# Kernel tuning notes

Hardware: AMD Instinct MI355X
Metric: run time of the kernel (lower is better)

The kernel has to match this reference:

```python
import jax, jax.numpy as jnp
import numpy as np

EPS = 1e-5
NUM_HEADS = 8
KEY_DEPTH = 128   # base_filters * key_expansion
VAL_DEPTH = 256   # base_filters * value_expansion
C_IN = 256


def conv1x1(x, w):
    # x: [N, Cin, L], w: [Cout, Cin] (1x1 conv, no bias)
    return jnp.einsum('oc,ncl->nol', w, x)


def group_norm1(x, w, b, eps=EPS):
    # torch GroupNorm(1, C) on [N, C, L]: normalize over (C, L) per sample,
    # per-channel affine.
    mu = jnp.mean(x, axis=(1, 2), keepdims=True)
    var = jnp.var(x, axis=(1, 2), keepdims=True)
    xn = (x - mu) * jax.lax.rsqrt(var + eps)
    return xn * w[None, :, None] + b[None, :, None]


def layer_norm_last2(x, eps=EPS):
    # freshly-constructed nn.LayerNorm([A, B]): weight=1, bias=0 -> pure norm
    mu = jnp.mean(x, axis=(-2, -1), keepdims=True)
    var = jnp.var(x, axis=(-2, -1), keepdims=True)
    return (x - mu) * jax.lax.rsqrt(var + eps)


def gelu(x):
    return jax.nn.gelu(x, approximate=False)  # torch F.gelu default (erf)


def setup_inputs() -> dict:
    key = jax.random.key(0)
    ks = jax.random.split(key, 16)
    N, L = 8, 1024
    qkv_out = 2 * KEY_DEPTH + VAL_DEPTH  # 512

    def w(k, shape, std=0.02):
        return jax.random.normal(k, shape, jnp.float32) * std

    def gw(k, c):
        return 1.0 + 0.1 * jax.random.normal(k, (c,), jnp.float32)

    return {
        'f': jax.random.normal(ks[0], (N, C_IN, L), jnp.float32),
        'w_z': w(ks[1], (C_IN, C_IN), np.sqrt(2.0 / C_IN)),
        'gz_w': gw(ks[2], C_IN), 'gz_b': w(ks[3], (C_IN,)),
        'w_qkv': w(ks[4], (qkv_out, C_IN), C_IN ** -0.5),
        'gq_w': gw(ks[5], qkv_out), 'gq_b': w(ks[6], (qkv_out,)),
        'w_out': w(ks[7], (C_IN, VAL_DEPTH), np.sqrt(2.0 / VAL_DEPTH)),
        'go_w': gw(ks[8], C_IN), 'go_b': w(ks[9], (C_IN,)),
        'w_ffn1': w(ks[10], (2 * C_IN, C_IN), np.sqrt(2.0 / C_IN)),
        'g1_w': gw(ks[11], 2 * C_IN), 'g1_b': w(ks[12], (2 * C_IN,)),
        'w_ffn2': w(ks[13], (C_IN, 2 * C_IN), np.sqrt(1.0 / C_IN)),
        'g2_w': gw(ks[14], C_IN), 'g2_b': w(ks[15], (C_IN,)),
    }


def reference(f, w_z, gz_w, gz_b, w_qkv, gq_w, gq_b, w_out, go_w, go_b,
              w_ffn1, g1_w, g1_b, w_ffn2, g2_w, g2_b):
    N, C, L = f.shape
    H = NUM_HEADS

    z = gelu(group_norm1(conv1x1(gelu(f), w_z), gz_w, gz_b))
    qkv = group_norm1(conv1x1(z, w_qkv), gq_w, gq_b)
    q, k, v = jnp.split(qkv, [KEY_DEPTH, 2 * KEY_DEPTH], axis=1)
    q = q.reshape(N, H, KEY_DEPTH // H, L)
    k = k.reshape(N, H, KEY_DEPTH // H, L)
    v = v.reshape(N, H, VAL_DEPTH // H, L)

    # [N, H, L, L] similarity, no scaling, then LayerNorm over full LxL map
    logits = jnp.einsum('nhcl,nhcm->nhlm', q, k)
    logits = layer_norm_last2(logits)

    # scatter-mask: diagonal -> -inf for every head
    eye = jnp.eye(L, dtype=bool)[None, None]  # [1,1,L,L]
    logits = jnp.where(eye, -jnp.inf, logits)

    attn = jax.nn.softmax(logits.astype(jnp.float32), axis=-1)
    attn = jnp.where(jnp.isnan(attn), 0.0, attn)

    out = jnp.einsum('nhlm,nhdm->nhdl', attn, v).reshape(N, VAL_DEPTH, L)
    out = gelu(layer_norm_last2(out))  # LayerNorm([C_v, L]), fresh params

    out = group_norm1(conv1x1(out, w_out), go_w, go_b)
    f = gelu(f + out)

    h = gelu(group_norm1(conv1x1(f, w_ffn1), g1_w, g1_b))
    h = group_norm1(conv1x1(h, w_ffn2), g2_w, g2_b)
    return gelu(f + h)
```

## Files before the change

kernel.cpp:

```cpp
#include <hip/hip_runtime.h>

#define LSEQ 1024

typedef __attribute__((ext_vector_type(8))) short bf16x8;
typedef __attribute__((ext_vector_type(4))) float f32x4;

__device__ __forceinline__ float gelu_f(float x){
    return 0.5f*x*(1.0f+erff(x*0.7071067811865476f));
}

__device__ __forceinline__ unsigned cvtpk(float lo, float hi){
    unsigned r;
    asm("v_cvt_pk_bf16_f32 %0, %1, %2" : "=v"(r) : "v"(lo), "v"(hi));
    return r;
}

__global__ __launch_bounds__(256,2) void prologue(
    const float* __restrict__ w0, const float* __restrict__ w1,
    const float* __restrict__ w2, const float* __restrict__ w3,
    const float* __restrict__ w4, unsigned short* __restrict__ wdst,
    const float* __restrict__ f, unsigned short* __restrict__ t0,
    float* __restrict__ stats, float* __restrict__ covs,
    unsigned* __restrict__ kmaxu)
{
    __shared__ float T[64][68];
    int b = blockIdx.x;
    int tid = threadIdx.x;

    if(b < 512){
        int ltile = (b&15)*64, ctile = ((b>>4)&3)*64, n = b>>6;
        const float* s = f + (size_t)n*256*LSEQ;
        int cl = tid>>4, l4 = (tid&15)*4;
        #pragma unroll
        for(int p=0;p<4;p++){
            int c_loc = p*16 + cl;
            float4 v = *(const float4*)&s[(size_t)(ctile+c_loc)*LSEQ + ltile + l4];
            float4 t;
            t.x = gelu_f(v.x); t.y = gelu_f(v.y); t.z = gelu_f(v.z); t.w = gelu_f(v.w);
            *(float4*)&T[c_loc][l4] = t;
        }
        __syncthreads();
        int l_loc = tid>>2, cg = (tid&3)*16;
        uint4 o0, o1;
        o0.x = cvtpk(T[cg+0][l_loc],  T[cg+1][l_loc]);
        o0.y = cvtpk(T[cg+2][l_loc],  T[cg+3][l_loc]);
        o0.z = cvtpk(T[cg+4][l_loc],  T[cg+5][l_loc]);
        o0.w = cvtpk(T[cg+6][l_loc],  T[cg+7][l_loc]);
        o1.x = cvtpk(T[cg+8][l_loc],  T[cg+9][l_loc]);
        o1.y = cvtpk(T[cg+10][l_loc], T[cg+11][l_loc]);
        o1.z = cvtpk(T[cg+12][l_loc], T[cg+13][l_loc]);
        o1.w = cvtpk(T[cg+14][l_loc], T[cg+15][l_loc]);
        unsigned short* d = t0 + (size_t)n*LSEQ*256 + (size_t)(ltile+l_loc)*256 + ctile + cg;
        *(uint4*)d = o0;
        *(uint4*)(d+8) = o1;
    } else if(b < 1024){
        int idx4 = (b-512)*256 + tid;
        const float* src; int off4;
        if(idx4 < 16384){ src=w0; off4=idx4; }
        else if(idx4 < 49152){ src=w1; off4=idx4-16384; }
        else if(idx4 < 65536){ src=w2; off4=idx4-49152; }
        else if(idx4 < 98304){ src=w3; off4=idx4-65536; }
        else { src=w4; off4=idx4-98304; }
        float4 v = ((const float4*)src)[off4];
        uint2 p; p.x = cvtpk(v.x,v.y); p.y = cvtpk(v.z,v.w);
        ((uint2*)wdst)[idx4] = p;
    } else if(b == 1024){
        if(tid < 64) ((float4*)stats)[tid] = (float4){0.f,0.f,0.f,0.f};
        if(tid >= 64 && tid < 80) ((uint4*)kmaxu)[tid-64] = (uint4){0,0,0,0};
    } else {
        int i = (b-1025)*256 + tid;
        ((float4*)covs)[i] = (float4){0.f,0.f,0.f,0.f};
    }
}

__global__ __launch_bounds__(256,2) void xform_bf16(
    const float* __restrict__ src, const float* __restrict__ res,
    const float* __restrict__ stats,
    const float* __restrict__ gw, const float* __restrict__ gb,
    float cnt_inv, int C, unsigned short* __restrict__ dst)
{
    __shared__ float T[64][68];
    int n = blockIdx.z;
    int ltile = blockIdx.x*64, ctile = blockIdx.y*64;
    int tid = threadIdx.x;

    float mu=0.f, istd=1.f;
    if(stats){
        float s1 = stats[2*n], s2 = stats[2*n+1];
        mu = s1*cnt_inv;
        istd = rsqrtf(s2*cnt_inv - mu*mu + 1e-5f);
    }
    const float* s = src + (size_t)n*C*LSEQ;
    const float* r = res ? res + (size_t)n*C*LSEQ : nullptr;

    int cl = tid>>4, l4 = (tid&15)*4;
    #pragma unroll
    for(int p=0;p<4;p++){
        int c_loc = p*16 + cl;
        int c = ctile + c_loc;
        float w_ = 1.f, b_ = 0.f;
        if(stats){ w_ = istd; b_ = -mu*istd; }
        if(gw){ b_ = gb[c] + b_*gw[c]; w_ *= gw[c]; }
        float4 v = *(const float4*)&s[(size_t)c*LSEQ + ltile + l4];
        float4 t;
        t.x = v.x*w_+b_; t.y = v.y*w_+b_; t.z = v.z*w_+b_; t.w = v.w*w_+b_;
        if(r){
            float4 rv = *(const float4*)&r[(size_t)c*LSEQ + ltile + l4];
            t.x += rv.x; t.y += rv.y; t.z += rv.z; t.w += rv.w;
        }
        t.x = gelu_f(t.x); t.y = gelu_f(t.y); t.z = gelu_f(t.z); t.w = gelu_f(t.w);
        *(float4*)&T[c_loc][l4] = t;
    }
    __syncthreads();

    int l_loc = tid>>2, cg = (tid&3)*16;
    uint4 o0, o1;
    o0.x = cvtpk(T[cg+0][l_loc],  T[cg+1][l_loc]);
    o0.y = cvtpk(T[cg+2][l_loc],  T[cg+3][l_loc]);
    o0.z = cvtpk(T[cg+4][l_loc],  T[cg+5][l_loc]);
    o0.w = cvtpk(T[cg+6][l_loc],  T[cg+7][l_loc]);
    o1.x = cvtpk(T[cg+8][l_loc],  T[cg+9][l_loc]);
    o1.y = cvtpk(T[cg+10][l_loc], T[cg+11][l_loc]);
    o1.z = cvtpk(T[cg+12][l_loc], T[cg+13][l_loc]);
    o1.w = cvtpk(T[cg+14][l_loc], T[cg+15][l_loc]);
    unsigned short* d = dst + (size_t)n*LSEQ*C + (size_t)(ltile+l_loc)*C + ctile + cg;
    *(uint4*)d = o0;
    *(uint4*)(d+8) = o1;
}

__global__ __launch_bounds__(256,4) void gemm_bf16(
    const unsigned short* __restrict__ Abf,
    const unsigned short* __restrict__ Bbf,
    float* __restrict__ C,
    int M, int K,
    float* __restrict__ out_stats)
{
    __shared__ short Bs[64*264];

    int tid = threadIdx.x;
    int n = blockIdx.z, n0 = blockIdx.x*64, m0 = blockIdx.y*64;
    int wave = tid>>6, lane = tid&63;
    int col = lane&15, quad = lane>>4;
    int srow = tid>>2, sks = (tid&3)*8;

    const unsigned short* apt = Abf + (size_t)(m0+wave*16+col)*K + quad*8;
    const unsigned short* bpt = Bbf + ((size_t)n*LSEQ + n0+srow)*K + sks;

    f32x4 acc[4];
    #pragma unroll
    for(int t=0;t<4;t++) acc[t] = (f32x4){0.f,0.f,0.f,0.f};

    for(int kp=0; kp<K; kp+=256){
        __syncthreads();
        uint4 bw[8];
        #pragma unroll
        for(int i=0;i<8;i++) bw[i] = *(const uint4*)(bpt + kp + i*32);
        #pragma unroll
        for(int i=0;i<8;i++) *(uint4*)&Bs[srow*264 + sks + i*32] = bw[i];
        __syncthreads();

        #pragma unroll
        for(int kc=0;kc<8;kc++){
            bf16x8 af = *(const bf16x8*)(apt + kp + kc*32);
            #pragma unroll
            for(int t=0;t<4;t++){
                bf16x8 bf = *(bf16x8*)&Bs[(t*16+col)*264 + kc*32 + quad*8];
                acc[t] = __builtin_amdgcn_mfma_f32_16x16x32_bf16(af, bf, acc[t], 0,0,0);
            }
        }
    }

    __syncthreads();
    size_t cbase = (size_t)n*M*LSEQ;
    float lsum=0.f, lsq=0.f;
    #pragma unroll
    for(int t=0;t<4;t++){
        #pragma unroll
        for(int r2=0;r2<4;r2++){
            int m = m0 + wave*16 + quad*4 + r2;
            int l = n0 + t*16 + col;
            float v = acc[t][r2];
            C[cbase + (size_t)m*LSEQ + l] = v;
            lsum += v; lsq += v*v;
        }
    }
    #pragma unroll
    for(int d=1;d<64;d<<=1){
        lsum += __shfl_xor(lsum, d);
        lsq  += __shfl_xor(lsq,  d);
    }
    float* scr = (float*)Bs;
    if(lane==0){ scr[wave] = lsum; scr[8+wave] = lsq; }
    __syncthreads();
    if(tid==0){
        atomicAdd(&out_stats[2*n],   (scr[0]+scr[1])+(scr[2]+scr[3]));
        atomicAdd(&out_stats[2*n+1], (scr[8]+scr[9])+(scr[10]+scr[11]));
    }
}

__global__ __launch_bounds__(256,4) void gemm_bf16_m128(
    const unsigned short* __restrict__ Abf,
    const unsigned short* __restrict__ Bbf,
    float* __restrict__ C,
    int M, int K,
    float* __restrict__ out_stats)
{
    __shared__ short Bs[64*264];

    int tid = threadIdx.x;
    int n = blockIdx.z, n0 = blockIdx.x*64, m0 = blockIdx.y*128;
    int wave = tid>>6, lane = tid&63;
    int col = lane&15, quad = lane>>4;
    int srow = tid>>2, sks = (tid&3)*8;

    const unsigned short* apt0 = Abf + (size_t)(m0+wave*32+col)*K + quad*8;
    const unsigned short* apt1 = apt0 + (size_t)16*K;
    const unsigned short* bpt = Bbf + ((size_t)n*LSEQ + n0+srow)*K + sks;

    f32x4 acc[2][4];
    #pragma unroll
    for(int mf=0;mf<2;mf++)
        #pragma unroll
        for(int t=0;t<4;t++) acc[mf][t] = (f32x4){0.f,0.f,0.f,0.f};

    for(int kp=0; kp<K; kp+=256){
        __syncthreads();
        uint4 bw[8];
        #pragma unroll
        for(int i=0;i<8;i++) bw[i] = *(const uint4*)(bpt + kp + i*32);
        #pragma unroll
        for(int i=0;i<8;i++) *(uint4*)&Bs[srow*264 + sks + i*32] = bw[i];
        __syncthreads();

        #pragma unroll
        for(int kc=0;kc<8;kc++){
            bf16x8 af0 = *(const bf16x8*)(apt0 + kp + kc*32);
            bf16x8 af1 = *(const bf16x8*)(apt1 + kp + kc*32);
            #pragma unroll
            for(int t=0;t<4;t++){
                bf16x8 bf = *(bf16x8*)&Bs[(t*16+col)*264 + kc*32 + quad*8];
                acc[0][t] = __builtin_amdgcn_mfma_f32_16x16x32_bf16(af0, bf, acc[0][t], 0,0,0);
                acc[1][t] = __builtin_amdgcn_mfma_f32_16x16x32_bf16(af1, bf, acc[1][t], 0,0,0);
            }
        }
    }

    __syncthreads();
    size_t cbase = (size_t)n*M*LSEQ;
    float lsum=0.f, lsq=0.f;
    #pragma unroll
    for(int mf=0;mf<2;mf++){
        #pragma unroll
        for(int t=0;t<4;t++){
            #pragma unroll
            for(int r2=0;r2<4;r2++){
                int m = m0 + wave*32 + mf*16 + quad*4 + r2;
                int l = n0 + t*16 + col;
                float v = acc[mf][t][r2];
                C[cbase + (size_t)m*LSEQ + l] = v;
                lsum += v; lsq += v*v;
            }
        }
    }
    #pragma unroll
    for(int d=1;d<64;d<<=1){
        lsum += __shfl_xor(lsum, d);
        lsq  += __shfl_xor(lsq,  d);
    }
    float* scr = (float*)Bs;
    if(lane==0){ scr[wave] = lsum; scr[8+wave] = lsq; }
    __syncthreads();
    if(tid==0){
        atomicAdd(&out_stats[2*n],   (scr[0]+scr[1])+(scr[2]+scr[3]));
        atomicAdd(&out_stats[2*n+1], (scr[8]+scr[9])+(scr[10]+scr[11]));
    }
}

__global__ __launch_bounds__(256,2) void head_cov(
    const float* __restrict__ qkv,
    const float* __restrict__ s_qkv,
    const float* __restrict__ gq_w, const float* __restrict__ gq_b,
    float* __restrict__ covq, float* __restrict__ covk,
    float* __restrict__ sumq, float* __restrict__ sumk,
    unsigned short* __restrict__ Qbf, unsigned short* __restrict__ Kbf,
    unsigned short* __restrict__ Vbf,
    float* __restrict__ qnorm, unsigned* __restrict__ kmaxu)
{
    __shared__ float Kq[16*132];
    __shared__ float Kk[16*132];
    int b = blockIdx.x;
    int head = b>>3, chunk = b&7;
    int n = head>>3, h = head&7;
    int tid = threadIdx.x;
    int m0 = chunk*128;

    float s1 = s_qkv[2*n], s2v = s_qkv[2*n+1];
    float mu  = s1*(1.f/524288.f);
    float var = s2v*(1.f/524288.f) - mu*mu;
    float istd = rsqrtf(var + 1e-5f);

    const float* base = qkv + (size_t)n*512*LSEQ;
    int m = tid&127, cg = tid>>7;
    #pragma unroll
    for(int cc=0;cc<8;cc++){
        int c = cg*8+cc;
        int chq = h*16+c, chk = 128+h*16+c;
        Kq[c*132+m] = (base[(size_t)chq*LSEQ+m0+m]-mu)*istd*gq_w[chq]+gq_b[chq];
        Kk[c*132+m] = (base[(size_t)chk*LSEQ+m0+m]-mu)*istd*gq_w[chk]+gq_b[chk];
    }

    {
        int d = tid>>3, mg = tid&7;
        int ch = 256 + h*32 + d;
        float vw = gq_w[ch]*istd, vb = gq_b[ch]-mu*istd*gq_w[ch];
        const float* vs = base + (size_t)ch*LSEQ + m0 + mg*16;
        float4 a0 = *(const float4*)&vs[0];
        float4 a1 = *(const float4*)&vs[4];
        float4 a2 = *(const float4*)&vs[8];
        float4 a3 = *(const float4*)&vs[12];
        uint4 p0, p1;
        p0.x = cvtpk(a0.x*vw+vb, a0.y*vw+vb);
        p0.y = cvtpk(a0.z*vw+vb, a0.w*vw+vb);
        p0.z = cvtpk(a1.x*vw+vb, a1.y*vw+vb);
        p0.w = cvtpk(a1.z*vw+vb, a1.w*vw+vb);
        p1.x = cvtpk(a2.x*vw+vb, a2.y*vw+vb);
        p1.y = cvtpk(a2.z*vw+vb, a2.w*vw+vb);
        p1.z = cvtpk(a3.x*vw+vb, a3.y*vw+vb);
        p1.w = cvtpk(a3.z*vw+vb, a3.w*vw+vb);
        unsigned short* dv = Vbf + ((size_t)head*32 + d)*1024 + m0 + mg*16;
        *(uint4*)dv = p0;
        *(uint4*)(dv+8) = p1;
    }
    __syncthreads();

    int i = tid>>4, j = tid&15;
    float q0=0,q1=0,q2=0,q3=0, k0=0,k1=0,k2=0,k3=0;
    for(int mm=0;mm<128;mm+=4){
        float4 qa = *(const float4*)&Kq[i*132+mm];
        float4 qb = *(const float4*)&Kq[j*132+mm];
        q0 += qa.x*qb.x; q1 += qa.y*qb.y; q2 += qa.z*qb.z; q3 += qa.w*qb.w;
        float4 ka = *(const float4*)&Kk[i*132+mm];
        float4 kb = *(const float4*)&Kk[j*132+mm];
        k0 += ka.x*kb.x; k1 += ka.y*kb.y; k2 += ka.z*kb.z; k3 += ka.w*kb.w;
    }
    atomicAdd(&covq[head*256 + i*16 + j], (q0+q1)+(q2+q3));
    atomicAdd(&covk[head*256 + i*16 + j], (k0+k1)+(k2+k3));

    if(i==0){
        float s=0.f;
        for(int mm=0;mm<128;mm+=4){
            float4 v = *(const float4*)&Kq[j*132+mm];
            s += (v.x+v.y)+(v.z+v.w);
        }
        atomicAdd(&sumq[head*16+j], s);
    }
    if(i==1){
        float s=0.f;
        for(int mm=0;mm<128;mm+=4){
            float4 v = *(const float4*)&Kk[j*132+mm];
            s += (v.x+v.y)+(v.z+v.w);
        }
        atomicAdd(&sumk[head*16+j], s);
    }

    {
        int mm2 = tid & 127;
        if(tid < 128){
            unsigned u[8]; float s2 = 0.f;
            #pragma unroll
            for(int c=0;c<16;c+=2){
                float a = Kq[c*132+mm2], b2 = Kq[(c+1)*132+mm2];
                s2 += a*a + b2*b2;
                u[c>>1] = cvtpk(a, b2);
            }
            unsigned short* dq = Qbf + ((size_t)head*1024 + m0 + mm2)*16;
            *(uint4*)dq     = *(uint4*)&u[0];
            *(uint4*)(dq+8) = *(uint4*)&u[4];
            qnorm[head*1024 + m0 + mm2] = s2;
        } else {
            unsigned u[8]; float s2 = 0.f;
            #pragma unroll
            for(int c=0;c<16;c+=2){
                float a = Kk[c*132+mm2], b2 = Kk[(c+1)*132+mm2];
                s2 += a*a + b2*b2;
                u[c>>1] = cvtpk(a, b2);
            }
            unsigned short* dk = Kbf + ((size_t)head*1024 + m0 + mm2)*16;
            *(uint4*)dk     = *(uint4*)&u[0];
            *(uint4*)(dk+8) = *(uint4*)&u[4];
            #pragma unroll
            for(int d=1;d<64;d<<=1) s2 = fmaxf(s2, __shfl_xor(s2, d));
            if((tid&63)==0) atomicMax(kmaxu + head, __float_as_uint(s2));
        }
    }
}

__global__ __launch_bounds__(256) void attn_kernel(
    const unsigned short* __restrict__ Qbf,
    const unsigned short* __restrict__ Kbf,
    const unsigned short* __restrict__ Vbf,
    const float* __restrict__ qnorm, const unsigned* __restrict__ kmaxu,
    const float* __restrict__ covq, const float* __restrict__ covk,
    const float* __restrict__ sumq, const float* __restrict__ sumk,
    float* __restrict__ out,
    float* __restrict__ out_stats)
{
    __shared__ short Qs[128*40];
    __shared__ short Ks[128*40];
    __shared__ short Vs[32*136];
    __shared__ short Ps[128*152];
    __shared__ float bounds_l[128];
    __shared__ float issum_l[128];
    __shared__ float sred4[4];

    int b = blockIdx.x;
    int head = b&63, rb = b>>6;
    int n = head>>3, h = head&7;
    int tid = threadIdx.x;
    int wv = tid>>6, lane = tid&63;
    int col = lane&15, quad = lane>>4;
    int l0 = rb*128;

    float ih;
    {
        float prod = covq[head*256+tid]*covk[head*256+tid];
        #pragma unroll
        for(int d=1;d<64;d<<=1) prod += __shfl_xor(prod, d);
        if(lane==0) sred4[wv] = prod;
        __syncthreads();
        if(tid==0){
            double S2 = (double)sred4[0] + (double)sred4[1]
                      + (double)sred4[2] + (double)sred4[3];
            double S1 = 0.0;
            for(int c=0;c<16;c++)
                S1 += (double)sumq[head*16+c]*(double)sumk[head*16+c];
            double cnt = 1048576.0;
            double mean = S1/cnt;
            double v2 = S2/cnt - mean*mean;
            if(v2 < 0.0) v2 = 0.0;
            sred4[0] = (float)(1.0/sqrt(v2 + 1e-5));
        }
        __syncthreads();
        ih = sred4[0];
    }
    float ihl = ih * 1.4426950408889634f;

    {
        uint4 z = {0,0,0,0};
        int row = tid>>1, hf = tid&1;
        *(uint4*)&Ks[row*40 + 16 + hf*8] = z;
        *(uint4*)&Qs[row*40 + 16 + hf*8] = z;
        const unsigned short* qsrc = Qbf + ((size_t)head*1024 + l0 + row)*16 + hf*8;
        *(uint4*)&Qs[row*40 + hf*8] = *(const uint4*)qsrc;
        if(tid < 128) bounds_l[tid] = sqrtf(qnorm[head*1024 + l0 + tid]);
    }
    float kmax = sqrtf(__uint_as_float(kmaxu[head]));
    __syncthreads();

    bf16x8 qf[2];
    float B2l[2]; int grow[2];
    #pragma unroll
    for(int t=0;t<2;t++){
        int rl = (2*wv+t)*16 + col;
        qf[t] = *(bf16x8*)&Qs[rl*40 + quad*8];
        B2l[t] = bounds_l[rl]*kmax*ihl;
        grow[t] = l0 + rl;
    }

    int krow = tid>>1, khalf = tid&1;
    const unsigned short* ksrc = Kbf + ((size_t)head*1024 + krow)*16 + khalf*8;
    int vdd = tid>>3, vmg = tid&7;
    const unsigned short* vsrc = Vbf + ((size_t)head*32 + vdd)*1024 + vmg*16;

    f32x4 acc[2][2];
    #pragma unroll
    for(int t=0;t<2;t++){ acc[t][0]=(f32x4){0,0,0,0}; acc[t][1]=(f32x4){0,0,0,0}; }
    float ssum[2] = {0.f,0.f};
    const f32x4 zero4 = {0.f,0.f,0.f,0.f};

    uint4 kreg = *(const uint4*)ksrc;
    uint4 vr0  = *(const uint4*)vsrc;
    uint4 vr1  = *(const uint4*)(vsrc + 8);

    for(int mc=0;mc<8;mc++){
        int M0 = mc*128;
        *(uint4*)&Ks[krow*40 + khalf*8]    = kreg;
        *(uint4*)&Vs[vdd*136 + vmg*16]     = vr0;
        *(uint4*)&Vs[vdd*136 + vmg*16 + 8] = vr1;
        __syncthreads();

        if(mc < 7){
            kreg = *(const uint4*)(ksrc + (size_t)(M0+128)*16);
            vr0  = *(const uint4*)(vsrc + M0+128);
            vr1  = *(const uint4*)(vsrc + M0+136);
        }

        __builtin_amdgcn_s_setprio(1);
        bool dg = (mc == rb);
        #pragma unroll
        for(int mt=0;mt<8;mt++){
            bf16x8 ak = *(bf16x8*)&Ks[(mt*16+col)*40 + quad*8];
            #pragma unroll
            for(int t=0;t<2;t++){
                f32x4 sc = __builtin_amdgcn_mfma_f32_16x16x32_bf16(ak, qf[t], zero4, 0,0,0);
                float pr[4];
                #pragma unroll
                for(int r=0;r<4;r++)
                    pr[r] = exp2f(fmaf(sc[r], ihl, -B2l[t]));
                if(dg){
                    int mbase = M0 + mt*16 + quad*4;
                    #pragma unroll
                    for(int r=0;r<4;r++)
                        if(mbase + r == grow[t]) pr[r] = 0.f;
                }
                ssum[t] += (pr[0]+pr[1])+(pr[2]+pr[3]);
                uint2 pw;
                pw.x = cvtpk(pr[0],pr[1]); pw.y = cvtpk(pr[2],pr[3]);
                *(uint2*)&Ps[((2*wv+t)*16+col)*152 + mt*16 + quad*4] = pw;
            }
        }
        #pragma unroll
        for(int kk=0;kk<4;kk++){
            bf16x8 bv0 = *(bf16x8*)&Vs[( col)*136 + kk*32 + quad*8];
            bf16x8 bv1 = *(bf16x8*)&Vs[(16+col)*136 + kk*32 + quad*8];
            #pragma unroll
            for(int t=0;t<2;t++){
                bf16x8 ap = *(bf16x8*)&Ps[((2*wv+t)*16+col)*152 + kk*32 + quad*8];
                acc[t][0] = __builtin_amdgcn_mfma_f32_16x16x32_bf16(ap, bv0, acc[t][0], 0,0,0);
                acc[t][1] = __builtin_amdgcn_mfma_f32_16x16x32_bf16(ap, bv1, acc[t][1], 0,0,0);
            }
        }
        __builtin_amdgcn_s_setprio(0);
        __syncthreads();
    }

    #pragma unroll
    for(int t=0;t<2;t++){
        float v = ssum[t];
        v += __shfl_xor(v,16);
        v += __shfl_xor(v,32);
        if(quad==0) issum_l[(2*wv+t)*16+col] = v;
    }
    __syncthreads();
    if(tid<128) issum_l[tid] = 1.f/issum_l[tid];
    __syncthreads();

    float* ep = (float*)Ps;
    #pragma unroll
    for(int t=0;t<2;t++)
        #pragma unroll
        for(int dt=0;dt<2;dt++)
            *(f32x4*)&ep[(dt*16+col)*132 + (2*wv+t)*16 + quad*4] = acc[t][dt];
    __syncthreads();

    float lsum=0.f, lsq=0.f;
    size_t obase = (size_t)n*262144 + (size_t)h*32*LSEQ + l0;
    #pragma unroll
    for(int t=0;t<16;t++){
        int idx = t*256 + tid;
        int d = idx>>7, row = idx&127;
        float y = ep[d*132+row]*issum_l[row];
        out[obase + (size_t)d*LSEQ + row] = y;
        lsum += y; lsq += y*y;
    }
    float* red = (float*)Ks;
    red[tid]=lsum; red[256+tid]=lsq;
    __syncthreads();
    for(int s=128;s>0;s>>=1){
        if(tid<s){ red[tid]+=red[tid+s]; red[256+tid]+=red[256+tid+s]; }
        __syncthreads();
    }
    if(tid==0){
        atomicAdd(&out_stats[2*n],   red[0]);
        atomicAdd(&out_stats[2*n+1], red[256]);
    }
}

__global__ __launch_bounds__(256) void ew_final(
    const float* __restrict__ f, const float* __restrict__ x,
    const float* __restrict__ h2,
    const float* __restrict__ sx, const float* __restrict__ sh,
    const float* __restrict__ go_w, const float* __restrict__ go_b,
    const float* __restrict__ g2_w, const float* __restrict__ g2_b,
    float* __restrict__ out)
{
    int idx = blockIdx.x*256 + threadIdx.x;
    int n = idx >> 16;
    int c = (idx >> 8) & 255;
    float mux, isx, muh, ish;
    {
        float s1 = sx[2*n], s2 = sx[2*n+1];
        mux = s1*(1.f/262144.f);
        isx = rsqrtf(s2*(1.f/262144.f) - mux*mux + 1e-5f);
        float t1 = sh[2*n], t2 = sh[2*n+1];
        muh = t1*(1.f/262144.f);
        ish = rsqrtf(t2*(1.f/262144.f) - muh*muh + 1e-5f);
    }
    float wo = go_w[c]*isx, bo = go_b[c]-mux*isx*go_w[c];
    float w2 = g2_w[c]*ish, b2 = g2_b[c]-muh*ish*g2_w[c];
    float4 xv = ((const float4*)x)[idx];
    float4 fv = ((const float4*)f)[idx];
    float4 hv = ((const float4*)h2)[idx];
    float4 ov;
    float f1;
    f1 = gelu_f(fv.x + xv.x*wo+bo); ov.x = gelu_f(f1 + hv.x*w2+b2);
    f1 = gelu_f(fv.y + xv.y*wo+bo); ov.y = gelu_f(f1 + hv.y*w2+b2);
    f1 = gelu_f(fv.z + xv.z*wo+bo); ov.z = gelu_f(f1 + hv.z*w2+b2);
    f1 = gelu_f(fv.w + xv.w*wo+bo); ov.w = gelu_f(f1 + hv.w*w2+b2);
    ((float4*)out)[idx] = ov;
}

extern "C" void kernel_launch(void* const* d_in, const int* in_sizes, int n_in,
                              void* d_out, int out_size, void* d_ws, size_t ws_size,
                              hipStream_t stream) {
    const float* f     = (const float*)d_in[0];
    const float* w_z   = (const float*)d_in[1];
    const float* gz_w  = (const float*)d_in[2];
    const float* gz_b  = (const float*)d_in[3];
    const float* w_qkv = (const float*)d_in[4];
    const float* gq_w  = (const float*)d_in[5];
    const float* gq_b  = (const float*)d_in[6];
    const float* w_out = (const float*)d_in[7];
    const float* go_w  = (const float*)d_in[8];
    const float* go_b  = (const float*)d_in[9];
    const float* w_f1  = (const float*)d_in[10];
    const float* g1_w  = (const float*)d_in[11];
    const float* g1_b  = (const float*)d_in[12];
    const float* w_f2  = (const float*)d_in[13];
    const float* g2_w  = (const float*)d_in[14];
    const float* g2_b  = (const float*)d_in[15];

    float* ws = (float*)d_ws;
    float* stats = ws;
    float* s_z    = stats + 0;
    float* s_qkv  = stats + 16;
    float* s_attn = stats + 32;
    float* s_x    = stats + 48;
    float* s_h1   = stats + 64;
    float* s_h2   = stats + 80;

    float* qkvF = ws + 256;
    float* z0F  = qkvF + 4194304;
    float* xF   = z0F + 2097152;
    unsigned short* t0 = (unsigned short*)(xF + 2097152);
    unsigned short* t1 = t0 + 2097152;
    unsigned short* wp = t1 + 2097152;
    unsigned short* t4 = (unsigned short*)z0F;
    unsigned short* wp_z   = wp;
    unsigned short* wp_qkv = wp + 65536;
    unsigned short* wp_out = wp + 196608;
    unsigned short* wp_f1  = wp + 262144;
    unsigned short* wp_f2  = wp + 393216;

    float* covq = xF;
    float* covk = xF + 16384;
    float* sumq = xF + 32768;
    float* sumk = xF + 33792;
    float* qnorm = xF + 34816;
    unsigned* kmaxu = (unsigned*)(xF + 100352);

    unsigned short* Qbf = t0;
    unsigned short* Kbf = t0 + 1048576;
    unsigned short* Vbf = t1;

    float* outp = (float*)d_out;

    dim3 blk(256);
    prologue<<<1059,blk,0,stream>>>(w_z, w_qkv, w_out, w_f1, w_f2, wp,
        f, t0, stats, covq, kmaxu);
    gemm_bf16<<<dim3(16,4,8),blk,0,stream>>>(wp_z, t0, z0F, 256, 256, s_z);
    xform_bf16<<<dim3(16,4,8),blk,0,stream>>>(z0F, nullptr, s_z, gz_w, gz_b,
        1.f/262144.f, 256, t1);
    gemm_bf16_m128<<<dim3(16,4,8),blk,0,stream>>>(wp_qkv, t1, qkvF, 512, 256, s_qkv);
    head_cov<<<512,blk,0,stream>>>(qkvF, s_qkv, gq_w, gq_b, covq, covk, sumq, sumk,
        Qbf, Kbf, Vbf, qnorm, kmaxu);
    attn_kernel<<<512,blk,0,stream>>>(Qbf, Kbf, Vbf, qnorm, kmaxu,
        covq, covk, sumq, sumk, z0F, s_attn);
    xform_bf16<<<dim3(16,4,8),blk,0,stream>>>(z0F, nullptr, s_attn, nullptr, nullptr,
        1.f/262144.f, 256, t0);
    gemm_bf16<<<dim3(16,4,8),blk,0,stream>>>(wp_out, t0, xF, 256, 256, s_x);
    xform_bf16<<<dim3(16,4,8),blk,0,stream>>>(xF, f, s_x, go_w, go_b,
        1.f/262144.f, 256, t1);
    gemm_bf16_m128<<<dim3(16,4,8),blk,0,stream>>>(wp_f1, t1, qkvF, 512, 256, s_h1);
    xform_bf16<<<dim3(16,8,8),blk,0,stream>>>(qkvF, nullptr, s_h1, g1_w, g1_b,
        1.f/524288.f, 512, t4);
    gemm_bf16<<<dim3(16,4,8),blk,0,stream>>>(wp_f2, t4, qkvF, 256, 512, s_h2);
    ew_final<<<2048,blk,0,stream>>>(f, xF, qkvF, s_x, s_h2,
        go_w, go_b, g2_w, g2_b, outp);
}
```

Before: 279.4 us.

## Fuse norm+GELU+bf16 transpose staging into GEMM B-tile loads

Removes the separate xform_bf16 passes and the gelu prologue transpose. Each GEMM now reads the fp32 activation directly, applies the group-norm affine, optional residual and GELU, and transposes through shared memory into the bf16 B tile. This saves several launches and the write and read of the bf16 intermediates. In exchange, every M-tile block recomputes GELU/erf for the same B columns (4x or 2x redundancy), adds extra barriers and LDS, and occupancy drops to 3 blocks per CU.

```diff
diff --git a/kernel.cpp b/kernel.cpp
--- a/kernel.cpp
+++ b/kernel.cpp
@@ -15,46 +15,66 @@
     return r;
 }
 
+__device__ __forceinline__ void stage_B_fused(
+    short* Bs, float* T,
+    const float* __restrict__ src, const float* __restrict__ res,
+    const float* __restrict__ gw, const float* __restrict__ gb,
+    float mu, float istd, bool has_stats,
+    int n0, int kp, int tid)
+{
+    int cl = tid>>4, l4 = (tid&15)*4;
+    int l_loc = tid>>2, cg = (tid&3)*16;
+    #pragma unroll
+    for(int sub=0; sub<4; sub++){
+        int cbase = kp + sub*64;
+        float4 tv[4];
+        #pragma unroll
+        for(int p=0;p<4;p++){
+            int c = cbase + p*16 + cl;
+            float w_ = 1.f, b_ = 0.f;
+            if(has_stats){ w_ = istd; b_ = -mu*istd; }
+            if(gw){ b_ = gb[c] + b_*gw[c]; w_ *= gw[c]; }
+            float4 v = *(const float4*)&src[(size_t)c*LSEQ + n0 + l4];
+            float4 t;
+            t.x = v.x*w_+b_; t.y = v.y*w_+b_; t.z = v.z*w_+b_; t.w = v.w*w_+b_;
+            if(res){
+                float4 rv = *(const float4*)&res[(size_t)c*LSEQ + n0 + l4];
+                t.x += rv.x; t.y += rv.y; t.z += rv.z; t.w += rv.w;
+            }
+            t.x = gelu_f(t.x); t.y = gelu_f(t.y); t.z = gelu_f(t.z); t.w = gelu_f(t.w);
+            tv[p] = t;
+        }
+        __syncthreads();
+        #pragma unroll
+        for(int p=0;p<4;p++) *(float4*)&T[(p*16+cl)*68 + l4] = tv[p];
+        __syncthreads();
+        uint4 o0, o1;
+        o0.x = cvtpk(T[(cg+0)*68+l_loc],  T[(cg+1)*68+l_loc]);
+        o0.y = cvtpk(T[(cg+2)*68+l_loc],  T[(cg+3)*68+l_loc]);
+        o0.z = cvtpk(T[(cg+4)*68+l_loc],  T[(cg+5)*68+l_loc]);
+        o0.w = cvtpk(T[(cg+6)*68+l_loc],  T[(cg+7)*68+l_loc]);
+        o1.x = cvtpk(T[(cg+8)*68+l_loc],  T[(cg+9)*68+l_loc]);
+        o1.y = cvtpk(T[(cg+10)*68+l_loc], T[(cg+11)*68+l_loc]);
+        o1.z = cvtpk(T[(cg+12)*68+l_loc], T[(cg+13)*68+l_loc]);
+        o1.w = cvtpk(T[(cg+14)*68+l_loc], T[(cg+15)*68+l_loc]);
+        *(uint4*)&Bs[l_loc*264 + sub*64 + cg]     = o0;
+        *(uint4*)&Bs[l_loc*264 + sub*64 + cg + 8] = o1;
+    }
+    __syncthreads();
+}
+
 __global__ __launch_bounds__(256,2) void prologue(
     const float* __restrict__ w0, const float* __restrict__ w1,
     const float* __restrict__ w2, const float* __restrict__ w3,
     const float* __restrict__ w4, unsigned short* __restrict__ wdst,
-    const float* __restrict__ f, unsigned short* __restrict__ t0,
     float* __restrict__ stats, float* __restrict__ covs,
     unsigned* __restrict__ kmaxu)
 {
-    __shared__ float T[64][68];
     int b = blockIdx.x;
     int tid = threadIdx.x;
 
     if(b < 512){
-        int ltile = (b&15)*64, ctile = ((b>>4)&3)*64, n = b>>6;
-        const float* s = f + (size_t)n*256*LSEQ;
-        int cl = tid>>4, l4 = (tid&15)*4;
-        #pragma unroll
-        for(int p=0;p<4;p++){
-            int c_loc = p*16 + cl;
-            float4 v = *(const float4*)&s[(size_t)(ctile+c_loc)*LSEQ + ltile + l4];
-            float4 t;
-            t.x = gelu_f(v.x); t.y = gelu_f(v.y); t.z = gelu_f(v.z); t.w = gelu_f(v.w);
-            *(float4*)&T[c_loc][l4] = t;
-        }
-        __syncthreads();
-        int l_loc = tid>>2, cg = (tid&3)*16;
-        uint4 o0, o1;
-        o0.x = cvtpk(T[cg+0][l_loc],  T[cg+1][l_loc]);
-        o0.y = cvtpk(T[cg+2][l_loc],  T[cg+3][l_loc]);
-        o0.z = cvtpk(T[cg+4][l_loc],  T[cg+5][l_loc]);
-        o0.w = cvtpk(T[cg+6][l_loc],  T[cg+7][l_loc]);
-        o1.x = cvtpk(T[cg+8][l_loc],  T[cg+9][l_loc]);
-        o1.y = cvtpk(T[cg+10][l_loc], T[cg+11][l_loc]);
-        o1.z = cvtpk(T[cg+12][l_loc], T[cg+13][l_loc]);
-        o1.w = cvtpk(T[cg+14][l_loc], T[cg+15][l_loc]);
-        unsigned short* d = t0 + (size_t)n*LSEQ*256 + (size_t)(ltile+l_loc)*256 + ctile + cg;
-        *(uint4*)d = o0;
-        *(uint4*)(d+8) = o1;
-    } else if(b < 1024){
-        int idx4 = (b-512)*256 + tid;
+        int idx4 = b*256 + tid;
         const float* src; int off4;
         if(idx4 < 16384){ src=w0; off4=idx4; }
         else if(idx4 < 49152){ src=w1; off4=idx4-16384; }
@@ -64,100 +84,50 @@
         float4 v = ((const float4*)src)[off4];
         uint2 p; p.x = cvtpk(v.x,v.y); p.y = cvtpk(v.z,v.w);
         ((uint2*)wdst)[idx4] = p;
-    } else if(b == 1024){
+    } else if(b == 512){
         if(tid < 64) ((float4*)stats)[tid] = (float4){0.f,0.f,0.f,0.f};
         if(tid >= 64 && tid < 80) ((uint4*)kmaxu)[tid-64] = (uint4){0,0,0,0};
     } else {
-        int i = (b-1025)*256 + tid;
+        int i = (b-513)*256 + tid;
         ((float4*)covs)[i] = (float4){0.f,0.f,0.f,0.f};
     }
 }
 
-__global__ __launch_bounds__(256,2) void xform_bf16(
-    const float* __restrict__ src, const float* __restrict__ res,
-    const float* __restrict__ stats,
+__global__ __launch_bounds__(256,3) void gemm_fused(
+    const unsigned short* __restrict__ Abf,
+    const float* __restrict__ srcF, const float* __restrict__ resF,
+    const float* __restrict__ in_stats, float cnt_inv, int Csrc,
     const float* __restrict__ gw, const float* __restrict__ gb,
-    float cnt_inv, int C, unsigned short* __restrict__ dst)
-{
-    __shared__ float T[64][68];
-    int n = blockIdx.z;
-    int ltile = blockIdx.x*64, ctile = blockIdx.y*64;
-    int tid = threadIdx.x;
-
-    float mu=0.f, istd=1.f;
-    if(stats){
-        float s1 = stats[2*n], s2 = stats[2*n+1];
-        mu = s1*cnt_inv;
-        istd = rsqrtf(s2*cnt_inv - mu*mu + 1e-5f);
-    }
-    const float* s = src + (size_t)n*C*LSEQ;
-    const float* r = res ? res + (size_t)n*C*LSEQ : nullptr;
-
-    int cl = tid>>4, l4 = (tid&15)*4;
-    #pragma unroll
-    for(int p=0;p<4;p++){
-        int c_loc = p*16 + cl;
-        int c = ctile + c_loc;
-        float w_ = 1.f, b_ = 0.f;
-        if(stats){ w_ = istd; b_ = -mu*istd; }
-        if(gw){ b_ = gb[c] + b_*gw[c]; w_ *= gw[c]; }
-        float4 v = *(const float4*)&s[(size_t)c*LSEQ + ltile + l4];
-        float4 t;
-        t.x = v.x*w_+b_; t.y = v.y*w_+b_; t.z = v.z*w_+b_; t.w = v.w*w_+b_;
-        if(r){
-            float4 rv = *(const float4*)&r[(size_t)c*LSEQ + ltile + l4];
-            t.x += rv.x; t.y += rv.y; t.z += rv.z; t.w += rv.w;
-        }
-        t.x = gelu_f(t.x); t.y = gelu_f(t.y); t.z = gelu_f(t.z); t.w = gelu_f(t.w);
-        *(float4*)&T[c_loc][l4] = t;
-    }
-    __syncthreads();
-
-    int l_loc = tid>>2, cg = (tid&3)*16;
-    uint4 o0, o1;
-    o0.x = cvtpk(T[cg+0][l_loc],  T[cg+1][l_loc]);
-    o0.y = cvtpk(T[cg+2][l_loc],  T[cg+3][l_loc]);
-    o0.z = cvtpk(T[cg+4][l_loc],  T[cg+5][l_loc]);
-    o0.w = cvtpk(T[cg+6][l_loc],  T[cg+7][l_loc]);
-    o1.x = cvtpk(T[cg+8][l_loc],  T[cg+9][l_loc]);
-    o1.y = cvtpk(T[cg+10][l_loc], T[cg+11][l_loc]);
-    o1.z = cvtpk(T[cg+12][l_loc], T[cg+13][l_loc]);
-    o1.w = cvtpk(T[cg+14][l_loc], T[cg+15][l_loc]);
-    unsigned short* d = dst + (size_t)n*LSEQ*C + (size_t)(ltile+l_loc)*C + ctile + cg;
-    *(uint4*)d = o0;
-    *(uint4*)(d+8) = o1;
-}
-
-__global__ __launch_bounds__(256,4) void gemm_bf16(
-    const unsigned short* __restrict__ Abf,
-    const unsigned short* __restrict__ Bbf,
     float* __restrict__ C,
     int M, int K,
     float* __restrict__ out_stats)
 {
     __shared__ short Bs[64*264];
+    __shared__ float T[64*68];
 
     int tid = threadIdx.x;
     int n = blockIdx.z, n0 = blockIdx.x*64, m0 = blockIdx.y*64;
     int wave = tid>>6, lane = tid&63;
     int col = lane&15, quad = lane>>4;
-    int srow = tid>>2, sks = (tid&3)*8;
+
+    float mu=0.f, istd=1.f;
+    bool has_stats = (in_stats != nullptr);
+    if(has_stats){
+        float s1 = in_stats[2*n], s2 = in_stats[2*n+1];
+        mu = s1*cnt_inv;
+        istd = rsqrtf(s2*cnt_inv - mu*mu + 1e-5f);
+    }
+    const float* src = srcF + (size_t)n*Csrc*LSEQ;
+    const float* res = resF ? resF + (size_t)n*Csrc*LSEQ : nullptr;
 
     const unsigned short* apt = Abf + (size_t)(m0+wave*16+col)*K + quad*8;
-    const unsigned short* bpt = Bbf + ((size_t)n*LSEQ + n0+srow)*K + sks;
 
     f32x4 acc[4];
     #pragma unroll
     for(int t=0;t<4;t++) acc[t] = (f32x4){0.f,0.f,0.f,0.f};
 
     for(int kp=0; kp<K; kp+=256){
-        __syncthreads();
-        uint4 bw[8];
-        #pragma unroll
-        for(int i=0;i<8;i++) bw[i] = *(const uint4*)(bpt + kp + i*32);
-        #pragma unroll
-        for(int i=0;i<8;i++) *(uint4*)&Bs[srow*264 + sks + i*32] = bw[i];
-        __syncthreads();
+        stage_B_fused(Bs, T, src, res, gw, gb, mu, istd, has_stats, n0, kp, tid);
 
         #pragma unroll
         for(int kc=0;kc<8;kc++){
@@ -198,24 +168,35 @@
     }
 }
 
-__global__ __launch_bounds__(256,4) void gemm_bf16_m128(
+__global__ __launch_bounds__(256,3) void gemm_fused_m128(
     const unsigned short* __restrict__ Abf,
-    const unsigned short* __restrict__ Bbf,
+    const float* __restrict__ srcF, const float* __restrict__ resF,
+    const float* __restrict__ in_stats, float cnt_inv, int Csrc,
+    const float* __restrict__ gw, const float* __restrict__ gb,
     float* __restrict__ C,
     int M, int K,
     float* __restrict__ out_stats)
 {
     __shared__ short Bs[64*264];
+    __shared__ float T[64*68];
 
     int tid = threadIdx.x;
     int n = blockIdx.z, n0 = blockIdx.x*64, m0 = blockIdx.y*128;
     int wave = tid>>6, lane = tid&63;
     int col = lane&15, quad = lane>>4;
-    int srow = tid>>2, sks = (tid&3)*8;
+
+    float mu=0.f, istd=1.f;
+    bool has_stats = (in_stats != nullptr);
+    if(has_stats){
+        float s1 = in_stats[2*n], s2 = in_stats[2*n+1];
+        mu = s1*cnt_inv;
+        istd = rsqrtf(s2*cnt_inv - mu*mu + 1e-5f);
+    }
+    const float* src = srcF + (size_t)n*Csrc*LSEQ;
+    const float* res = resF ? resF + (size_t)n*Csrc*LSEQ : nullptr;
 
     const unsigned short* apt0 = Abf + (size_t)(m0+wave*32+col)*K + quad*8;
     const unsigned short* apt1 = apt0 + (size_t)16*K;
-    const unsigned short* bpt = Bbf + ((size_t)n*LSEQ + n0+srow)*K + sks;
 
     f32x4 acc[2][4];
     #pragma unroll
@@ -224,13 +205,7 @@
         for(int t=0;t<4;t++) acc[mf][t] = (f32x4){0.f,0.f,0.f,0.f};
 
     for(int kp=0; kp<K; kp+=256){
-        __syncthreads();
-        uint4 bw[8];
-        #pragma unroll
-        for(int i=0;i<8;i++) bw[i] = *(const uint4*)(bpt + kp + i*32);
-        #pragma unroll
-        for(int i=0;i<8;i++) *(uint4*)&Bs[srow*264 + sks + i*32] = bw[i];
-        __syncthreads();
+        stage_B_fused(Bs, T, src, res, gw, gb, mu, istd, has_stats, n0, kp, tid);
 
         #pragma unroll
         for(int kc=0;kc<8;kc++){
@@ -645,7 +620,6 @@
     unsigned short* t0 = (unsigned short*)(xF + 2097152);
     unsigned short* t1 = t0 + 2097152;
     unsigned short* wp = t1 + 2097152;
-    unsigned short* t4 = (unsigned short*)z0F;
     unsigned short* wp_z   = wp;
     unsigned short* wp_qkv = wp + 65536;
     unsigned short* wp_out = wp + 196608;
@@ -666,25 +640,22 @@
     float* outp = (float*)d_out;
 
     dim3 blk(256);
-    prologue<<<1059,blk,0,stream>>>(w_z, w_qkv, w_out, w_f1, w_f2, wp,
-        f, t0, stats, covq, kmaxu);
-    gemm_bf16<<<dim3(16,4,8),blk,0,stream>>>(wp_z, t0, z0F, 256, 256, s_z);
-    xform_bf16<<<dim3(16,4,8),blk,0,stream>>>(z0F, nullptr, s_z, gz_w, gz_b,
-        1.f/262144.f, 256, t1);
-    gemm_bf16_m128<<<dim3(16,4,8),blk,0,stream>>>(wp_qkv, t1, qkvF, 512, 256, s_qkv);
+    prologue<<<547,blk,0,stream>>>(w_z, w_qkv, w_out, w_f1, w_f2, wp,
+        stats, covq, kmaxu);
+    gemm_fused<<<dim3(16,4,8),blk,0,stream>>>(wp_z, f, nullptr,
+        nullptr, 0.f, 256, nullptr, nullptr, z0F, 256, 256, s_z);
+    gemm_fused_m128<<<dim3(16,4,8),blk,0,stream>>>(wp_qkv, z0F, nullptr,
+        s_z, 1.f/262144.f, 256, gz_w, gz_b, qkvF, 512, 256, s_qkv);
     head_cov<<<512,blk,0,stream>>>(qkvF, s_qkv, gq_w, gq_b, covq, covk, sumq, sumk,
         Qbf, Kbf, Vbf, qnorm, kmaxu);
     attn_kernel<<<512,blk,0,stream>>>(Qbf, Kbf, Vbf, qnorm, kmaxu,
         covq, covk, sumq, sumk, z0F, s_attn);
-    xform_bf16<<<dim3(16,4,8),blk,0,stream>>>(z0F, nullptr, s_attn, nullptr, nullptr,
-        1.f/262144.f, 256, t0);
-    gemm_bf16<<<dim3(16,4,8),blk,0,stream>>>(wp_out, t0, xF, 256, 256, s_x);
-    xform_bf16<<<dim3(16,4,8),blk,0,stream>>>(xF, f, s_x, go_w, go_b,
-        1.f/262144.f, 256, t1);
-    gemm_bf16_m128<<<dim3(16,4,8),blk,0,stream>>>(wp_f1, t1, qkvF, 512, 256, s_h1);
-    xform_bf16<<<dim3(16,8,8),blk,0,stream>>>(qkvF, nullptr, s_h1, g1_w, g1_b,
-        1.f/524288.f, 512, t4);
-    gemm_bf16<<<dim3(16,4,8),blk,0,stream>>>(wp_f2, t4, qkvF, 256, 512, s_h2);
-    ew_final<<<2048,blk,0,stream>>>(f, xF, qkvF, s_x, s_h2,
+    gemm_fused<<<dim3(16,4,8),blk,0,stream>>>(wp_out, z0F, nullptr,
+        s_attn, 1.f/262144.f, 256, nullptr, nullptr, xF, 256, 256, s_x);
+    gemm_fused_m128<<<dim3(16,4,8),blk,0,stream>>>(wp_f1, xF, f,
+        s_x, 1.f/262144.f, 256, go_w, go_b, qkvF, 512, 256, s_h1);
+    gemm_fused<<<dim3(16,4,8),blk,0,stream>>>(wp_f2, qkvF, nullptr,
+        s_h1, 1.f/524288.f, 512, g1_w, g1_b, z0F, 256, 512, s_h2);
+    ew_final<<<2048,blk,0,stream>>>(f, xF, z0F, s_x, s_h2,
         go_w, go_b, g2_w, g2_b, outp);
 }
```

After: 325.6 us. 1.17x slower.
